# Kernel optimization log

Hardware: AMD Instinct MI355X
Metric: run time of the kernel (lower is better)

Reference implementation:

```python
import jax, jax.numpy as jnp
import numpy as np

D, H1, H2, OUT = 1024, 4096, 4096, 1


def _tanh_jet(a0, a1, a2):
    # 2nd-order Taylor-mode push-through of tanh:
    # u0 = tanh(a0); u1 = sech^2(a0)*a1; u2 = sech^2(a0)*a2 - 2*tanh(a0)*sech^2(a0)*a1^2
    u0 = jnp.tanh(a0)
    s = 1.0 - u0 * u0
    u1 = s * a1
    u2 = s * a2 - 2.0 * u0 * s * (a1 * a1)
    return u0, u1, u2


def setup_inputs() -> dict:
    key = jax.random.key(0)
    ks = jax.random.split(key, 7)
    x = jax.random.normal(ks[0], (D,), dtype=jnp.float32)
    # Kaiming-like scaling so tanh stays in its nonlinear regime
    W1 = jax.random.normal(ks[1], (H1, D), dtype=jnp.float32) / np.sqrt(D)
    b1 = jax.random.normal(ks[2], (H1,), dtype=jnp.float32) * 0.01
    W2 = jax.random.normal(ks[3], (H2, H1), dtype=jnp.float32) / np.sqrt(H1)
    b2 = jax.random.normal(ks[4], (H2,), dtype=jnp.float32) * 0.01
    W3 = jax.random.normal(ks[5], (OUT, H2), dtype=jnp.float32) / np.sqrt(H2)
    b3 = jax.random.normal(ks[6], (OUT,), dtype=jnp.float32) * 0.01
    return {"x": x, "W1": W1, "b1": b1, "W2": W2, "b2": b2, "W3": W3, "b3": b3}


def reference(x, W1, b1, W2, b2, W3, b3):
    # propagated simultaneously over all D basis tangent vectors (vectorized vmap).
    d = x.shape[0]
    X1 = jnp.eye(d, dtype=x.dtype)            # [D, D] basis tangents; x2 = 0
    # layer 1 (linear): primal broadcasts over the tangent batch
    a0 = x @ W1.T + b1                         # [H1]
    a1 = X1 @ W1.T                             # [D, H1]
    a2 = jnp.zeros_like(a1)                    # second input coefficient is zero
    u0, u1, u2 = _tanh_jet(a0, a1, a2)
    # layer 2 (linear)
    z0 = u0 @ W2.T + b2                        # [H2]
    z1 = u1 @ W2.T                             # [D, H2]
    z2 = u2 @ W2.T                             # [D, H2]
    v0, v1, v2 = _tanh_jet(z0, z1, z2)
    # layer 3 (linear); F2[i] = e_i^T H_f(x) e_i
    F2 = v2 @ W3.T                             # [D, 1]
    return F2.sum(0)                           # [1] = trace(H_f) = Laplacian
```

## Files before the change

### kernel.cpp

```cpp
#include <hip/hip_runtime.h>
#include <math.h>

#define DD 1024
#define HH1 4096
#define HH2 4096

typedef __attribute__((ext_vector_type(4))) int i32x4;
typedef __attribute__((ext_vector_type(4))) float f32x4;
typedef unsigned short ushort_t;

#define WS_FAST_BYTES 42008576ull
#define K4_LDS_BYTES (131072 + 64)

#define DEQ (1.f / 524288.f)

__device__ inline void wave_reduce2(float& a, float& b) {
  #pragma unroll
  for (int off = 32; off > 0; off >>= 1) {
    a += __shfl_down(a, off, 64);
    b += __shfl_down(b, off, 64);
  }
}

__device__ inline int q8(float v, float scale) {
  return (int)rintf(fminf(fmaxf(v * scale, -127.f), 127.f));
}
__device__ inline unsigned pk8(int a, int b, int c, int d) {
  return (a & 255) | ((b & 255) << 8) | ((c & 255) << 16) | ((d & 255) << 24);
}

__device__ inline void gl_lds16(const void* g, void* l) {
  __builtin_amdgcn_global_load_lds(
      (const __attribute__((address_space(1))) unsigned int*)g,
      (__attribute__((address_space(3))) unsigned int*)l, 16, 0, 0);
}

#define TPB 1040
__global__ __launch_bounds__(256) void kA3_l1t(
    const float* __restrict__ W1, const float* __restrict__ x,
    const float* __restrict__ b1, float* __restrict__ u0,
    float* __restrict__ q, char* __restrict__ Bp) {
  __shared__ __align__(16) char T[16 * TPB];
  const int tid = threadIdx.x;
  const int h0 = blockIdx.x * 16;
  const int r = tid >> 4;
  const int c = tid & 15;
  const float4* rp = (const float4*)(W1 + (size_t)(h0 + r) * DD);
  const float4* x4 = (const float4*)x;
  float dot = 0.f, sq = 0.f;
  #pragma unroll
  for (int j = 0; j < 16; ++j) {
    const int f = c + j * 16;
    float4 wv = rp[f];
    float4 xv = x4[f];
    dot += wv.x * xv.x + wv.y * xv.y + wv.z * xv.z + wv.w * xv.w;
    sq  += wv.x * wv.x + wv.y * wv.y + wv.z * wv.z + wv.w * wv.w;
    unsigned pk = pk8(q8(wv.x, 512.f), q8(wv.y, 512.f),
                      q8(wv.z, 512.f), q8(wv.w, 512.f));
    *(unsigned*)&T[r * TPB + f * 4] = pk;
  }
  #pragma unroll
  for (int off = 8; off > 0; off >>= 1) {
    dot += __shfl_down(dot, off, 16);
    sq  += __shfl_down(sq, off, 16);
  }
  if (c == 0) {
    float a0 = dot + b1[h0 + r];
    float u = tanhf(a0);
    float s = 1.f - u * u;
    u0[h0 + r] = u;
    q[h0 + r] = -2.f * u * s * sq;
  }
  __syncthreads();
  const int ip = tid * 4;
  unsigned R[16];
  #pragma unroll
  for (int rr = 0; rr < 16; ++rr)
    R[rr] = *(const unsigned*)&T[rr * TPB + ip];
  #pragma unroll
  for (int cc = 0; cc < 4; ++cc) {
    unsigned ow[4];
    #pragma unroll
    for (int wg = 0; wg < 4; ++wg) {
      ow[wg] = ((R[4 * wg] >> (8 * cc)) & 255u)
             | (((R[4 * wg + 1] >> (8 * cc)) & 255u) << 8)
             | (((R[4 * wg + 2] >> (8 * cc)) & 255u) << 16)
             | (((R[4 * wg + 3] >> (8 * cc)) & 255u) << 24);
    }
    *(uint4*)(Bp + (size_t)(ip + cc) * HH1 + h0) = *(const uint4*)ow;
  }
}

__global__ __launch_bounds__(256) void k0a_layer2conv(
    const float* __restrict__ W2, const float* __restrict__ b2,
    const float* __restrict__ W3, const float* __restrict__ u0,
    const float* __restrict__ q, char* __restrict__ Ap,
    float* __restrict__ cv, float* __restrict__ cd) {
  int g = blockIdx.x;
  int tid = threadIdx.x;
  const float4* row = (const float4*)(W2 + (size_t)g * HH1);
  const float4* u4 = (const float4*)u0;
  const float4* q4 = (const float4*)q;
  float4 w[4], u[4], qq[4];
  #pragma unroll
  for (int it = 0; it < 4; ++it) w[it] = row[tid + it * 256];
  #pragma unroll
  for (int it = 0; it < 4; ++it) u[it] = u4[tid + it * 256];
  #pragma unroll
  for (int it = 0; it < 4; ++it) qq[it] = q4[tid + it * 256];
  float zacc = 0.f, dacc = 0.f;
  #pragma unroll
  for (int it = 0; it < 4; ++it) {
    const int j = tid + it * 256;
    float4 sv;
    sv.x = 1.f - u[it].x * u[it].x;
    sv.y = 1.f - u[it].y * u[it].y;
    sv.z = 1.f - u[it].z * u[it].z;
    sv.w = 1.f - u[it].w * u[it].w;
    zacc += w[it].x * u[it].x + w[it].y * u[it].y +
            w[it].z * u[it].z + w[it].w * u[it].w;
    dacc += w[it].x * qq[it].x + w[it].y * qq[it].y +
            w[it].z * qq[it].z + w[it].w * qq[it].w;
    unsigned pk = pk8(q8(w[it].x * sv.x, 1024.f), q8(w[it].y * sv.y, 1024.f),
                      q8(w[it].z * sv.z, 1024.f), q8(w[it].w * sv.w, 1024.f));
    *(unsigned*)(Ap + (size_t)g * HH1 + j * 4) = pk;
  }
  wave_reduce2(zacc, dacc);
  __shared__ float lds[8];
  int lane = tid & 63, wid = tid >> 6;
  if (lane == 0) { lds[wid * 2] = zacc; lds[wid * 2 + 1] = dacc; }
  __syncthreads();
  if (tid == 0) {
    float z = lds[0] + lds[2] + lds[4] + lds[6] + b2[g];
    float d = lds[1] + lds[3] + lds[5] + lds[7];
    float v = tanhf(z);
    float t = 1.f - v * v;
    float c = W3[g] * t;
    cv[g] = c * v;
    cd[g] = c * d;
  }
}

__global__ __launch_bounds__(512) void k4_i8(
    const char* __restrict__ Ap, const char* __restrict__ Bp,
    const float* __restrict__ cv, float* __restrict__ P) {
  extern __shared__ __align__(16) char smem[];
  char* const Ab0 = smem;
  char* const Bb0 = smem + 65536;
  float* const red = (float*)(smem + 131072);

  const int tid = threadIdx.x;
  const int lane = tid & 63;
  const int wave = tid >> 6;
  const int wm = wave >> 1;
  const int wn = wave & 1;
  const int l = blockIdx.x;
  const int xcd = l & 7;
  const int jj = l >> 3;
  const int g0 = (xcd * 4 + (jj & 3)) * 128;
  const int i0 = (jj >> 2) * 128;

  const int srow = lane >> 3;
  const int schunk = (lane & 7) ^ srow;
  const size_t agbase = (size_t)(g0 + srow) * HH1 + schunk * 16;
  const size_t bgbase = (size_t)(i0 + srow) * HH1 + schunk * 16;

  const int fr = lane & 15;
  const int fc = lane >> 4;
  const int rsw = fr & 7;

  i32x4 acc[2][4];
  const i32x4 zero = {0, 0, 0, 0};
  #pragma unroll
  for (int mt = 0; mt < 2; ++mt)
    #pragma unroll
    for (int nt = 0; nt < 4; ++nt) acc[mt][nt] = zero;

  #define STAGE_PAIR(tile, sub) do {                                        \
      const int buf_ = (tile) & 3;                                          \
      const int r0_ = wave * 16 + (sub) * 8;                                \
      const size_t koff_ = (size_t)(((tile) & 31) * 128);                   \
      gl_lds16(Ap + agbase + (size_t)r0_ * HH1 + koff_,                     \
               Ab0 + buf_ * 16384 + r0_ * 128);                             \
      gl_lds16(Bp + bgbase + (size_t)r0_ * HH1 + koff_,                     \
               Bb0 + buf_ * 16384 + r0_ * 128);                             \
    } while (0)

  STAGE_PAIR(0, 0); STAGE_PAIR(0, 1);
  STAGE_PAIR(1, 0); STAGE_PAIR(1, 1);
  STAGE_PAIR(2, 0); STAGE_PAIR(2, 1);

  for (int t = 0; t < 32; ++t) {
    const int buf = t & 3;
    const char* Abuf = Ab0 + buf * 16384;
    const char* Bbuf = Bb0 + buf * 16384;
    asm volatile("s_waitcnt vmcnt(8)" ::: "memory");
    __builtin_amdgcn_s_barrier();
    asm volatile("" ::: "memory");
    #pragma unroll
    for (int kk = 0; kk < 2; ++kk) {
      STAGE_PAIR(t + 3, kk);
      i32x4 af[2], bfv[4];
      #pragma unroll
      for (int mt = 0; mt < 2; ++mt) {
        const int row = wm * 32 + mt * 16 + fr;
        af[mt] = *(const i32x4*)(Abuf + row * 128 + (((kk * 4 + fc) ^ rsw) * 16));
      }
      #pragma unroll
      for (int nt = 0; nt < 4; ++nt) {
        const int row = wn * 64 + nt * 16 + fr;
        bfv[nt] = *(const i32x4*)(Bbuf + row * 128 + (((kk * 4 + fc) ^ rsw) * 16));
      }
      __builtin_amdgcn_s_setprio(1);
      #pragma unroll
      for (int mt = 0; mt < 2; ++mt)
        #pragma unroll
        for (int nt = 0; nt < 4; ++nt)
          acc[mt][nt] = __builtin_amdgcn_mfma_i32_16x16x64_i8(
              af[mt], bfv[nt], acc[mt][nt], 0, 0, 0);
      __builtin_amdgcn_s_setprio(0);
    }
    asm volatile("" ::: "memory");
    __builtin_amdgcn_s_barrier();
  }
  #undef STAGE_PAIR

  float part = 0.f;
  #pragma unroll
  for (int mt = 0; mt < 2; ++mt) {
    #pragma unroll
    for (int r = 0; r < 4; ++r) {
      const int g = g0 + wm * 32 + mt * 16 + fc * 4 + r;
      const float c = cv[g];
      float ss = 0.f;
      #pragma unroll
      for (int nt = 0; nt < 4; ++nt) {
        float v = (float)acc[mt][nt][r] * DEQ;
        ss += v * v;
      }
      part += c * ss;
    }
  }
  #pragma unroll
  for (int off = 32; off > 0; off >>= 1) part += __shfl_down(part, off, 64);
  if (lane == 0) red[wave] = part;
  __syncthreads();
  if (tid == 0) {
    float s = 0.f;
    #pragma unroll
    for (int w2 = 0; w2 < 8; ++w2) s += red[w2];
    P[l] = s;
  }
}

__global__ __launch_bounds__(256) void k5_final(
    const float* __restrict__ cd, const float* __restrict__ P,
    float* __restrict__ out) {
  int tid = threadIdx.x;
  float a = 0.f;
  for (int j = tid; j < HH2; j += 256) a += cd[j];
  float b = P[tid];
  float v = a - 2.f * b;
  #pragma unroll
  for (int off = 32; off > 0; off >>= 1) v += __shfl_down(v, off, 64);
  __shared__ float lds[4];
  int lane = tid & 63, wid = tid >> 6;
  if (lane == 0) lds[wid] = v;
  __syncthreads();
  if (tid == 0) out[0] = lds[0] + lds[1] + lds[2] + lds[3];
}


__global__ __launch_bounds__(256) void k1_slow(
    const float* __restrict__ W1, const float* __restrict__ x,
    const float* __restrict__ b1, float* __restrict__ u0,
    float* __restrict__ q, float* __restrict__ s_out,
    float* __restrict__ out) {
  int h = blockIdx.x;
  int tid = threadIdx.x;
  const float4* row = (const float4*)(W1 + (size_t)h * DD);
  const float4* x4 = (const float4*)x;
  float4 w = row[tid];
  float4 xv = x4[tid];
  float dot = w.x * xv.x + w.y * xv.y + w.z * xv.z + w.w * xv.w;
  float sq = w.x * w.x + w.y * w.y + w.z * w.z + w.w * w.w;
  wave_reduce2(dot, sq);
  __shared__ float lds[8];
  int lane = tid & 63, wid = tid >> 6;
  if (lane == 0) { lds[wid * 2] = dot; lds[wid * 2 + 1] = sq; }
  __syncthreads();
  if (tid == 0) {
    float dsum = lds[0] + lds[2] + lds[4] + lds[6];
    float rsum = lds[1] + lds[3] + lds[5] + lds[7];
    float a0 = dsum + b1[h];
    float u = tanhf(a0);
    float s = 1.f - u * u;
    u0[h] = u;
    s_out[h] = s;
    q[h] = -2.f * u * s * rsum;
    if (h == 0) out[0] = 0.f;
  }
}

__global__ __launch_bounds__(256) void k2_slow(
    const float* __restrict__ W2, const float* __restrict__ b2,
    const float* __restrict__ W3, const float* __restrict__ u0,
    const float* __restrict__ q, float* __restrict__ cv,
    float* __restrict__ out) {
  int g = blockIdx.x;
  int tid = threadIdx.x;
  const float4* row = (const float4*)(W2 + (size_t)g * HH1);
  const float4* u4 = (const float4*)u0;
  const float4* q4 = (const float4*)q;
  float zacc = 0.f, dacc = 0.f;
  for (int j = tid; j < HH1 / 4; j += 256) {
    float4 w = row[j];
    float4 u = u4[j];
    float4 qq = q4[j];
    zacc += w.x * u.x + w.y * u.y + w.z * u.z + w.w * u.w;
    dacc += w.x * qq.x + w.y * qq.y + w.z * qq.z + w.w * qq.w;
  }
  wave_reduce2(zacc, dacc);
  __shared__ float lds[8];
  int lane = tid & 63, wid = tid >> 6;
  if (lane == 0) { lds[wid * 2] = zacc; lds[wid * 2 + 1] = dacc; }
  __syncthreads();
  if (tid == 0) {
    float z = lds[0] + lds[2] + lds[4] + lds[6] + b2[g];
    float d = lds[1] + lds[3] + lds[5] + lds[7];
    float v = tanhf(z);
    float t = 1.f - v * v;
    float c = W3[g] * t;
    cv[g] = c * v;
    atomicAdd(out, c * d);
  }
}

__global__ __launch_bounds__(256) void k4_slow(
    const float* __restrict__ W2, const float* __restrict__ W1,
    const float* __restrict__ s, const float* __restrict__ cv,
    float* __restrict__ out) {
  __shared__ float As[32][68];
  __shared__ float Bs[32][68];
  int tid = threadIdx.x;
  int g0 = blockIdx.y * 64;
  int i0 = blockIdx.x * 64;
  int tr = (tid / 16) * 4;
  int tc = (tid % 16) * 4;
  float acc[4][4] = {};
  for (int k0 = 0; k0 < HH1; k0 += 32) {
    for (int ll = tid; ll < (64 * 32 / 4); ll += 256) {
      int row = ll / 8;
      int c4 = ll % 8;
      float4 w = *(const float4*)(W2 + (size_t)(g0 + row) * HH1 + k0 + c4 * 4);
      float4 sv = *(const float4*)(s + k0 + c4 * 4);
      As[c4 * 4 + 0][row] = w.x * sv.x;
      As[c4 * 4 + 1][row] = w.y * sv.y;
      As[c4 * 4 + 2][row] = w.z * sv.z;
      As[c4 * 4 + 3][row] = w.w * sv.w;
    }
    for (int ll = tid; ll < (32 * 64 / 4); ll += 256) {
      int row = ll / 16;
      int c4 = ll % 16;
      float4 w = *(const float4*)(W1 + (size_t)(k0 + row) * DD + i0 + c4 * 4);
      *(float4*)&Bs[row][c4 * 4] = w;
    }
    __syncthreads();
    #pragma unroll
    for (int k = 0; k < 32; ++k) {
      float4 av = *(const float4*)&As[k][tr];
      float4 bv = *(const float4*)&Bs[k][tc];
      float a_[4] = {av.x, av.y, av.z, av.w};
      float b_[4] = {bv.x, bv.y, bv.z, bv.w};
      #pragma unroll
      for (int r = 0; r < 4; ++r)
        #pragma unroll
        for (int c = 0; c < 4; ++c)
          acc[r][c] += a_[r] * b_[c];
    }
    __syncthreads();
  }
  float contrib = 0.f;
  #pragma unroll
  for (int r = 0; r < 4; ++r) {
    float ss = acc[r][0] * acc[r][0] + acc[r][1] * acc[r][1] +
               acc[r][2] * acc[r][2] + acc[r][3] * acc[r][3];
    contrib += cv[g0 + tr + r] * ss;
  }
  #pragma unroll
  for (int off = 32; off > 0; off >>= 1) contrib += __shfl_down(contrib, off, 64);
  __shared__ float red[4];
  int lane = tid & 63, wid = tid >> 6;
  if (lane == 0) red[wid] = contrib;
  __syncthreads();
  if (tid == 0) atomicAdd(out, -2.f * (red[0] + red[1] + red[2] + red[3]));
}

extern "C" void kernel_launch(void* const* d_in, const int* in_sizes, int n_in,
                              void* d_out, int out_size, void* d_ws, size_t ws_size,
                              hipStream_t stream) {
  const float* x  = (const float*)d_in[0];
  const float* W1 = (const float*)d_in[1];
  const float* b1 = (const float*)d_in[2];
  const float* W2 = (const float*)d_in[3];
  const float* b2 = (const float*)d_in[4];
  const float* W3 = (const float*)d_in[5];
  float* out = (float*)d_out;
  float* ws = (float*)d_ws;

  if (ws_size >= WS_FAST_BYTES) {
    float* u0 = ws;
    float* q  = ws + 4096;
    float* cv = ws + 8192;
    float* cd = ws + 12288;
    float* P  = ws;
    char* Ap = (char*)d_ws + 65536;
    char* Bp = (char*)d_ws + 33619968;
    hipFuncSetAttribute((const void*)k4_i8,
                        hipFuncAttributeMaxDynamicSharedMemorySize,
                        K4_LDS_BYTES);
    hipLaunchKernelGGL(kA3_l1t, dim3(256), dim3(256), 0, stream,
                       W1, x, b1, u0, q, Bp);
    hipLaunchKernelGGL(k0a_layer2conv, dim3(HH2), dim3(256), 0, stream,
                       W2, b2, W3, u0, q, Ap, cv, cd);
    hipLaunchKernelGGL(k4_i8, dim3(256), dim3(512), K4_LDS_BYTES, stream,
                       Ap, Bp, cv, P);
    hipLaunchKernelGGL(k5_final, dim3(1), dim3(256), 0, stream, cd, P, out);
  } else {
    float* u0 = ws;
    float* q  = ws + 4096;
    float* s  = ws + 8192;
    float* cv = ws + 12288;
    hipLaunchKernelGGL(k1_slow, dim3(HH1), dim3(256), 0, stream,
                       W1, x, b1, u0, q, s, out);
    hipLaunchKernelGGL(k2_slow, dim3(HH2), dim3(256), 0, stream,
                       W2, b2, W3, u0, q, cv, out);
    hipLaunchKernelGGL(k4_slow, dim3(DD / 64, HH2 / 64), dim3(256), 0, stream,
                       W2, W1, s, cv, out);
  }
}
```

Baseline: 148.5 us.

## Load B fragments directly from global into registers, double-buffered, halving LDS use

The int8 GEMM kernel stops staging the B operand through LDS. Each wave now loads its B fragments straight from global memory into a register double buffer (b0/b1) one tile ahead, while A keeps its 4-stage LDS pipeline. This halves LDS footprint and LDS read traffic, but adds 32 VGPRs for B buffers and raises global load count, since B rows are read by both wm waves without LDS sharing. The vmcnt wait is retuned to match the new outstanding-load counts.

After: 198.8 us. 33.9% more time.

```diff
diff --git a/kernel.cpp b/kernel.cpp
--- a/kernel.cpp
+++ b/kernel.cpp
@@ -10,7 +10,7 @@
 typedef unsigned short ushort_t;
 
 #define WS_FAST_BYTES 42008576ull
-#define K4_LDS_BYTES (131072 + 64)
+#define K4B_LDS_BYTES (65536 + 64)
 
 #define DEQ (1.f / 524288.f)
 
@@ -141,13 +141,12 @@
   }
 }
 
-__global__ __launch_bounds__(512) void k4_i8(
+__global__ __launch_bounds__(512) void k4_i8b(
     const char* __restrict__ Ap, const char* __restrict__ Bp,
     const float* __restrict__ cv, float* __restrict__ P) {
   extern __shared__ __align__(16) char smem[];
   char* const Ab0 = smem;
-  char* const Bb0 = smem + 65536;
-  float* const red = (float*)(smem + 131072);
+  float* const red = (float*)(smem + 65536);
 
   const int tid = threadIdx.x;
   const int lane = tid & 63;
@@ -163,12 +162,16 @@
   const int srow = lane >> 3;
   const int schunk = (lane & 7) ^ srow;
   const size_t agbase = (size_t)(g0 + srow) * HH1 + schunk * 16;
-  const size_t bgbase = (size_t)(i0 + srow) * HH1 + schunk * 16;
 
   const int fr = lane & 15;
   const int fc = lane >> 4;
   const int rsw = fr & 7;
 
+  const char* bR0 = Bp + (size_t)(i0 + wn * 64 +  0 + fr) * HH1 + fc * 16;
+  const char* bR1 = Bp + (size_t)(i0 + wn * 64 + 16 + fr) * HH1 + fc * 16;
+  const char* bR2 = Bp + (size_t)(i0 + wn * 64 + 32 + fr) * HH1 + fc * 16;
+  const char* bR3 = Bp + (size_t)(i0 + wn * 64 + 48 + fr) * HH1 + fc * 16;
+
   i32x4 acc[2][4];
   const i32x4 zero = {0, 0, 0, 0};
   #pragma unroll
@@ -176,54 +179,84 @@
     #pragma unroll
     for (int nt = 0; nt < 4; ++nt) acc[mt][nt] = zero;
 
-  #define STAGE_PAIR(tile, sub) do {                                        \
+  i32x4 b0[8], b1[8];
+
+  #define STAGE_A(tile, sub) do {                                           \
       const int buf_ = (tile) & 3;                                          \
       const int r0_ = wave * 16 + (sub) * 8;                                \
       const size_t koff_ = (size_t)(((tile) & 31) * 128);                   \
       gl_lds16(Ap + agbase + (size_t)r0_ * HH1 + koff_,                     \
                Ab0 + buf_ * 16384 + r0_ * 128);                             \
-      gl_lds16(Bp + bgbase + (size_t)r0_ * HH1 + koff_,                     \
-               Bb0 + buf_ * 16384 + r0_ * 128);                             \
     } while (0)
 
-  STAGE_PAIR(0, 0); STAGE_PAIR(0, 1);
-  STAGE_PAIR(1, 0); STAGE_PAIR(1, 1);
-  STAGE_PAIR(2, 0); STAGE_PAIR(2, 1);
-
-  for (int t = 0; t < 32; ++t) {
-    const int buf = t & 3;
-    const char* Abuf = Ab0 + buf * 16384;
-    const char* Bbuf = Bb0 + buf * 16384;
-    asm volatile("s_waitcnt vmcnt(8)" ::: "memory");
-    __builtin_amdgcn_s_barrier();
-    asm volatile("" ::: "memory");
-    #pragma unroll
-    for (int kk = 0; kk < 2; ++kk) {
-      STAGE_PAIR(t + 3, kk);
-      i32x4 af[2], bfv[4];
-      #pragma unroll
-      for (int mt = 0; mt < 2; ++mt) {
-        const int row = wm * 32 + mt * 16 + fr;
-        af[mt] = *(const i32x4*)(Abuf + row * 128 + (((kk * 4 + fc) ^ rsw) * 16));
-      }
-      #pragma unroll
-      for (int nt = 0; nt < 4; ++nt) {
-        const int row = wn * 64 + nt * 16 + fr;
-        bfv[nt] = *(const i32x4*)(Bbuf + row * 128 + (((kk * 4 + fc) ^ rsw) * 16));
-      }
-      __builtin_amdgcn_s_setprio(1);
-      #pragma unroll
-      for (int mt = 0; mt < 2; ++mt)
-        #pragma unroll
-        for (int nt = 0; nt < 4; ++nt)
-          acc[mt][nt] = __builtin_amdgcn_mfma_i32_16x16x64_i8(
-              af[mt], bfv[nt], acc[mt][nt], 0, 0, 0);
-      __builtin_amdgcn_s_setprio(0);
-    }
-    asm volatile("" ::: "memory");
-    __builtin_amdgcn_s_barrier();
-  }
-  #undef STAGE_PAIR
+  #define LOADB(t, BN) do {                                                 \
+      const int kb_ = ((t) & 31) * 128;                                     \
+      BN[0] = *(const i32x4*)(bR0 + kb_);                                   \
+      BN[1] = *(const i32x4*)(bR0 + kb_ + 64);                              \
+      BN[2] = *(const i32x4*)(bR1 + kb_);                                   \
+      BN[3] = *(const i32x4*)(bR1 + kb_ + 64);                              \
+      BN[4] = *(const i32x4*)(bR2 + kb_);                                   \
+      BN[5] = *(const i32x4*)(bR2 + kb_ + 64);                              \
+      BN[6] = *(const i32x4*)(bR3 + kb_);                                   \
+      BN[7] = *(const i32x4*)(bR3 + kb_ + 64);                              \
+    } while (0)
+
+  #define K4_ITER(t, BC, BN) do {                                           \
+      asm volatile("s_waitcnt vmcnt(12)" ::: "memory");                     \
+      __builtin_amdgcn_s_barrier();                                         \
+      asm volatile("" ::: "memory");                                        \
+      LOADB((t) + 1, BN);                                                   \
+      STAGE_A((t) + 3, 0); STAGE_A((t) + 3, 1);                             \
+      {                                                                     \
+        const char* Abuf_ = Ab0 + ((t) & 3) * 16384;                        \
+        i32x4 af0_, af1_;                                                   \
+                                                                \
+        af0_ = *(const i32x4*)(Abuf_ + (wm * 32 +  0 + fr) * 128 +          \
+                               (((0 * 4 + fc) ^ rsw) * 16));                \
+        af1_ = *(const i32x4*)(Abuf_ + (wm * 32 + 16 + fr) * 128 +          \
+                               (((0 * 4 + fc) ^ rsw) * 16));                \
+        __builtin_amdgcn_s_setprio(1);                                      \
+        acc[0][0] = __builtin_amdgcn_mfma_i32_16x16x64_i8(af0_, BC[0], acc[0][0], 0, 0, 0); \
+        acc[0][1] = __builtin_amdgcn_mfma_i32_16x16x64_i8(af0_, BC[2], acc[0][1], 0, 0, 0); \
+        acc[0][2] = __builtin_amdgcn_mfma_i32_16x16x64_i8(af0_, BC[4], acc[0][2], 0, 0, 0); \
+        acc[0][3] = __builtin_amdgcn_mfma_i32_16x16x64_i8(af0_, BC[6], acc[0][3], 0, 0, 0); \
+        acc[1][0] = __builtin_amdgcn_mfma_i32_16x16x64_i8(af1_, BC[0], acc[1][0], 0, 0, 0); \
+        acc[1][1] = __builtin_amdgcn_mfma_i32_16x16x64_i8(af1_, BC[2], acc[1][1], 0, 0, 0); \
+        acc[1][2] = __builtin_amdgcn_mfma_i32_16x16x64_i8(af1_, BC[4], acc[1][2], 0, 0, 0); \
+        acc[1][3] = __builtin_amdgcn_mfma_i32_16x16x64_i8(af1_, BC[6], acc[1][3], 0, 0, 0); \
+        __builtin_amdgcn_s_setprio(0);                                      \
+                                                                \
+        af0_ = *(const i32x4*)(Abuf_ + (wm * 32 +  0 + fr) * 128 +          \
+                               (((1 * 4 + fc) ^ rsw) * 16));                \
+        af1_ = *(const i32x4*)(Abuf_ + (wm * 32 + 16 + fr) * 128 +          \
+                               (((1 * 4 + fc) ^ rsw) * 16));                \
+        __builtin_amdgcn_s_setprio(1);                                      \
+        acc[0][0] = __builtin_amdgcn_mfma_i32_16x16x64_i8(af0_, BC[1], acc[0][0], 0, 0, 0); \
+        acc[0][1] = __builtin_amdgcn_mfma_i32_16x16x64_i8(af0_, BC[3], acc[0][1], 0, 0, 0); \
+        acc[0][2] = __builtin_amdgcn_mfma_i32_16x16x64_i8(af0_, BC[5], acc[0][2], 0, 0, 0); \
+        acc[0][3] = __builtin_amdgcn_mfma_i32_16x16x64_i8(af0_, BC[7], acc[0][3], 0, 0, 0); \
+        acc[1][0] = __builtin_amdgcn_mfma_i32_16x16x64_i8(af1_, BC[1], acc[1][0], 0, 0, 0); \
+        acc[1][1] = __builtin_amdgcn_mfma_i32_16x16x64_i8(af1_, BC[3], acc[1][1], 0, 0, 0); \
+        acc[1][2] = __builtin_amdgcn_mfma_i32_16x16x64_i8(af1_, BC[5], acc[1][2], 0, 0, 0); \
+        acc[1][3] = __builtin_amdgcn_mfma_i32_16x16x64_i8(af1_, BC[7], acc[1][3], 0, 0, 0); \
+        __builtin_amdgcn_s_setprio(0);                                      \
+      }                                                                     \
+      asm volatile("" ::: "memory");                                        \
+      __builtin_amdgcn_s_barrier();                                         \
+    } while (0)
+
+  STAGE_A(0, 0); STAGE_A(0, 1);
+  STAGE_A(1, 0); STAGE_A(1, 1);
+  STAGE_A(2, 0); STAGE_A(2, 1);
+  LOADB(0, b0);
+
+  for (int tt = 0; tt < 32; tt += 2) {
+    K4_ITER(tt, b0, b1);
+    K4_ITER(tt + 1, b1, b0);
+  }
+  #undef K4_ITER
+  #undef LOADB
+  #undef STAGE_A
 
   float part = 0.f;
   #pragma unroll
@@ -243,6 +276,7 @@
   }
   #pragma unroll
   for (int off = 32; off > 0; off >>= 1) part += __shfl_down(part, off, 64);
+  asm volatile("s_waitcnt vmcnt(0)" ::: "memory");
   if (lane == 0) red[wave] = part;
   __syncthreads();
   if (tid == 0) {
@@ -416,14 +450,14 @@
     float* P  = ws;
     char* Ap = (char*)d_ws + 65536;
     char* Bp = (char*)d_ws + 33619968;
-    hipFuncSetAttribute((const void*)k4_i8,
+    hipFuncSetAttribute((const void*)k4_i8b,
                         hipFuncAttributeMaxDynamicSharedMemorySize,
-                        K4_LDS_BYTES);
+                        K4B_LDS_BYTES);
     hipLaunchKernelGGL(kA3_l1t, dim3(256), dim3(256), 0, stream,
                        W1, x, b1, u0, q, Bp);
     hipLaunchKernelGGL(k0a_layer2conv, dim3(HH2), dim3(256), 0, stream,
                        W2, b2, W3, u0, q, Ap, cv, cd);
-    hipLaunchKernelGGL(k4_i8, dim3(256), dim3(512), K4_LDS_BYTES, stream,
+    hipLaunchKernelGGL(k4_i8b, dim3(256), dim3(512), K4B_LDS_BYTES, stream,
                        Ap, Bp, cv, P);
     hipLaunchKernelGGL(k5_final, dim3(1), dim3(256), 0, stream, cd, P, out);
   } else {
```
